# Optimization experiments

Measured on AMD Instinct MI355X. Metric: run time of the kernel, lower is better.

Reference implementation:

```python
import jax, jax.numpy as jnp
import numpy as np

EPS = 1e-4  # softmax_kernel eps

def softmax_kernel(data, projection, is_query):
    # data: [b,h,n,d], projection: [m,d]
    d = data.shape[-1]
    m = projection.shape[0]
    data_normalizer = d ** -0.25
    ratio = m ** -0.5
    data_dash = jnp.einsum('bhnd,md->bhnm', data_normalizer * data, projection)
    diag_data = (jnp.sum(data ** 2, axis=-1) * 0.5 * data_normalizer ** 2)[..., None]  # [b,h,n,1]
    if is_query:
        stab = jnp.max(data_dash, axis=-1, keepdims=True)
    else:
        stab = jnp.max(data_dash)
    return ratio * (jnp.exp(data_dash - diag_data - stab) + EPS)

def linear_attention(q, k, v):
    # q,k: [b,h,n,m]; v: [b,h,n,e]
    k_cumsum = jnp.sum(k, axis=-2)                                  # [b,h,m]
    D_inv = 1.0 / jnp.einsum('bhnm,bhm->bhn', q, k_cumsum)          # [b,h,n]
    context = jnp.einsum('bhnm,bhne->bhme', k, v)                   # [b,h,m,e]
    return jnp.einsum('bhme,bhnm,bhn->bhne', context, q, D_inv)     # [b,h,n,e]

def setup_inputs() -> dict:
    key = jax.random.key(0)
    kq, kk, kv, kp = jax.random.split(key, 4)
    B, H, N, D = 4, 8, 4096, 64
    M = 266  # int(64 * ln(64))
    q = jax.random.normal(kq, (B, H, N, D), dtype=jnp.float32)
    k = jax.random.normal(kk, (B, H, N, D), dtype=jnp.float32)
    v = jax.random.normal(kv, (B, H, N, D), dtype=jnp.float32)
    # Gaussian random-feature projection (stand-in for orthogonal blocks; same math path)
    projection = jax.random.normal(kp, (M, D), dtype=jnp.float32)
    return {"q": q, "k": k, "v": v, "projection": projection}

def reference(q, k, v, projection):
    q_prime = softmax_kernel(q, projection, is_query=True)
    k_prime = softmax_kernel(k, projection, is_query=False)
    return linear_attention(q_prime, k_prime, v)
```

## Files before the change

kernel.cpp:

```cpp
#include <hip/hip_runtime.h>
#include <math.h>

#define NN 4096
#define DD 64
#define MM 266
#define MP 272
#define NORMZ 0.35355339059327379f
#define RATIO 0.06131393394849658f
#define EPSV 1e-4f
#define NEG_INF (-3.4e38f)
#define LSTR 72
#define GSTR 320

typedef __attribute__((ext_vector_type(8))) short bfrag;
typedef __attribute__((ext_vector_type(4))) float f32x4;

#define MFMA(a, b, c) __builtin_amdgcn_mfma_f32_16x16x32_bf16((a), (b), (c), 0, 0, 0)

__device__ inline ushort bf16rne(float x) {
    union { float f; unsigned u; } c; c.f = x;
    unsigned r = c.u + 0x7FFFu + ((c.u >> 16) & 1u);
    return (ushort)(r >> 16);
}
__device__ inline float bf2f(ushort h) {
    union { unsigned u; float f; } c; c.u = ((unsigned)h) << 16;
    return c.f;
}
__device__ inline void splitf(float x, ushort& h, ushort& l) {
    h = bf16rne(x);
    l = bf16rne(x - bf2f(h));
}
__device__ inline void pack8(const float4& a, const float4& b, bfrag& H, bfrag& L) {
    ushort h, l;
    splitf(a.x, h, l); H[0] = (short)h; L[0] = (short)l;
    splitf(a.y, h, l); H[1] = (short)h; L[1] = (short)l;
    splitf(a.z, h, l); H[2] = (short)h; L[2] = (short)l;
    splitf(a.w, h, l); H[3] = (short)h; L[3] = (short)l;
    splitf(b.x, h, l); H[4] = (short)h; L[4] = (short)l;
    splitf(b.y, h, l); H[5] = (short)h; L[5] = (short)l;
    splitf(b.z, h, l); H[6] = (short)h; L[6] = (short)l;
    splitf(b.w, h, l); H[7] = (short)h; L[7] = (short)l;
}

__global__ void proj_split(const float* __restrict__ proj,
                           ushort* __restrict__ pH, ushort* __restrict__ pL)
{
    int i = (blockIdx.x * 256 + threadIdx.x) * 4;
    int m = i >> 6;
    float4 x = (m < MM) ? *(const float4*)(proj + i) : make_float4(0.f, 0.f, 0.f, 0.f);
    ushort h0, l0, h1, l1, h2, l2, h3, l3;
    splitf(x.x, h0, l0); splitf(x.y, h1, l1); splitf(x.z, h2, l2); splitf(x.w, h3, l3);
    *(ushort4*)(pH + i) = make_ushort4(h0, h1, h2, h3);
    *(ushort4*)(pL + i) = make_ushort4(l0, l1, l2, l3);
}

__global__ void reduce_max_kernel(const float* __restrict__ partmax,
                                  float* __restrict__ stab, int n)
{
    __shared__ float sm[256];
    const int t = threadIdx.x;
    float mx = NEG_INF;
    for (int i = t; i < n; i += 256) mx = fmaxf(mx, partmax[i]);
    sm[t] = mx;
    __syncthreads();
    for (int s = 128; s > 0; s >>= 1) {
        if (t < s) sm[t] = fmaxf(sm[t], sm[t + s]);
        __syncthreads();
    }
    if (t == 0) *stab = sm[0];
}

__launch_bounds__(256, 2)
__global__ void kpass(const float* __restrict__ kin, const float* __restrict__ vin,
                      const ushort* __restrict__ pjH, const ushort* __restrict__ pjL,
                      float* __restrict__ ctxP, float* __restrict__ kcP,
                      float* __restrict__ pmax, float* __restrict__ vsum)
{
    __shared__ ushort dataH[64 * LSTR], dataLo[64 * LSTR];
    __shared__ ushort vTH[64 * LSTR], vTLo[64 * LSTR];
    __shared__ ushort r2H[64 * LSTR], r2Lo[64 * LSTR];
    __shared__ float diagS[64];
    __shared__ float kcS[MP];
    __shared__ float redS[4];
    __shared__ float vredS[DD];

    const int t = threadIdx.x;
    const int w = t >> 6;
    const int lane = t & 63;
    const int l15 = lane & 15;
    const int q = lane >> 4;
    const int hd = blockIdx.y;
    const int nb = blockIdx.x;

    kcS[t] = 0.f;
    if (t < 16) kcS[256 + t] = 0.f;
    if (t < DD) vredS[t] = 0.f;

    const f32x4 zf = {0.f, 0.f, 0.f, 0.f};
    f32x4 cacc[4][4];
    f32x4 cacc4 = zf;
    #pragma unroll
    for (int c = 0; c < 4; ++c)
        #pragma unroll
        for (int e = 0; e < 4; ++e) cacc[c][e] = zf;
    float bmaxl = NEG_INF;
    float4 vacc = make_float4(0.f, 0.f, 0.f, 0.f);

    #pragma unroll 1
    for (int st = 0; st < 4; ++st) {
        const int n0 = (nb << 8) + (st << 6);
        __syncthreads();

        const float* kb = kin + ((size_t)hd * NN + n0) * DD;
        #pragma unroll
        for (int j = 0; j < 4; ++j) {
            int i = (t + (j << 8)) << 2;
            int r = i >> 6, cc = i & 63;
            float4 x = *(const float4*)(kb + i);
            float x0 = x.x * NORMZ, x1 = x.y * NORMZ, x2 = x.z * NORMZ, x3 = x.w * NORMZ;
            ushort h0, l0, h1, l1, h2, l2, h3, l3;
            splitf(x0, h0, l0); splitf(x1, h1, l1); splitf(x2, h2, l2); splitf(x3, h3, l3);
            *(ushort4*)&dataH[r * LSTR + cc] = make_ushort4(h0, h1, h2, h3);
            *(ushort4*)&dataLo[r * LSTR + cc] = make_ushort4(l0, l1, l2, l3);
            float ss = x0 * x0 + x1 * x1 + x2 * x2 + x3 * x3;
            #pragma unroll
            for (int d = 1; d < 16; d <<= 1) ss += __shfl_xor(ss, d);
            if (l15 == 0) diagS[r] = 0.5f * ss;
        }
        const float* vb = vin + ((size_t)hd * NN + n0) * DD;
        #pragma unroll
        for (int j = 0; j < 4; ++j) {
            int i = (t + (j << 8)) << 2;
            int n = i >> 6, e = i & 63;
            float4 x = *(const float4*)(vb + i);
            vacc.x += x.x; vacc.y += x.y; vacc.z += x.z; vacc.w += x.w;
            ushort h, l;
            splitf(x.x, h, l); vTH[(e + 0) * LSTR + n] = h; vTLo[(e + 0) * LSTR + n] = l;
            splitf(x.y, h, l); vTH[(e + 1) * LSTR + n] = h; vTLo[(e + 1) * LSTR + n] = l;
            splitf(x.z, h, l); vTH[(e + 2) * LSTR + n] = h; vTLo[(e + 2) * LSTR + n] = l;
            splitf(x.w, h, l); vTH[(e + 3) * LSTR + n] = h; vTLo[(e + 3) * LSTR + n] = l;
        }
        __syncthreads();

        bfrag aH[2], aL[2];
        {
            const int row = (w << 4) + l15;
            aH[0] = *(const bfrag*)&dataH[row * LSTR + (q << 3)];
            aH[1] = *(const bfrag*)&dataH[row * LSTR + 32 + (q << 3)];
            aL[0] = *(const bfrag*)&dataLo[row * LSTR + (q << 3)];
            aL[1] = *(const bfrag*)&dataLo[row * LSTR + 32 + (q << 3)];
        }

        #pragma unroll
        for (int c = 0; c < 5; ++c) {
            const int mtiles = (c < 4) ? 4 : 1;
            const int m0 = c << 6;
            {
                const int tot = mtiles << 7;
                for (int idx = t; idx < tot; idx += 256) {
                    int i = idx << 3; int r = i >> 6, cc = i & 63;
                    *(uint4*)&r2H[r * LSTR + cc] = *(const uint4*)(pjH + ((m0 + r) << 6) + cc);
                    *(uint4*)&r2Lo[r * LSTR + cc] = *(const uint4*)(pjL + ((m0 + r) << 6) + cc);
                }
            }
            __syncthreads();

            f32x4 dd4[4];
            #pragma unroll
            for (int mt = 0; mt < 4; ++mt) {
                if (mt >= mtiles) break;
                const int mrow = (mt << 4) + l15;
                bfrag bH0 = *(const bfrag*)&r2H[mrow * LSTR + (q << 3)];
                bfrag bH1 = *(const bfrag*)&r2H[mrow * LSTR + 32 + (q << 3)];
                bfrag bL0 = *(const bfrag*)&r2Lo[mrow * LSTR + (q << 3)];
                bfrag bL1 = *(const bfrag*)&r2Lo[mrow * LSTR + 32 + (q << 3)];
                f32x4 a = zf;
                a = MFMA(aH[0], bL0, a);
                a = MFMA(aH[1], bL1, a);
                a = MFMA(aL[0], bH0, a);
                a = MFMA(aL[1], bH1, a);
                a = MFMA(aH[0], bH0, a);
                a = MFMA(aH[1], bH1, a);
                dd4[mt] = a;
            }
            #pragma unroll
            for (int mt = 0; mt < 4; ++mt) {
                if (mt >= mtiles) break;
                const int mg = m0 + (mt << 4) + l15;
                const bool valid = (mg < MM);
                ushort uh[4], ul[4];
                float csum = 0.f;
                #pragma unroll
                for (int reg = 0; reg < 4; ++reg) {
                    float dv = dd4[mt][reg];
                    float u = 0.f;
                    if (valid) {
                        bmaxl = fmaxf(bmaxl, dv);
                        u = __expf(dv - diagS[(w << 4) + (q << 2) + reg]);
                    }
                    csum += u;
                    splitf(u, uh[reg], ul[reg]);
                }
                *(ushort4*)&dataH[((mt << 4) + l15) * LSTR + (w << 4) + (q << 2)] =
                    make_ushort4(uh[0], uh[1], uh[2], uh[3]);
                *(ushort4*)&dataLo[((mt << 4) + l15) * LSTR + (w << 4) + (q << 2)] =
                    make_ushort4(ul[0], ul[1], ul[2], ul[3]);
                csum += __shfl_xor(csum, 16);
                csum += __shfl_xor(csum, 32);
                if (q == 0) atomicAdd(&kcS[mg], csum);
            }
            __syncthreads();

            if (c < 4) {
                const int mrow = (w << 4) + l15;
                bfrag uH0 = *(const bfrag*)&dataH[mrow * LSTR + (q << 3)];
                bfrag uH1 = *(const bfrag*)&dataH[mrow * LSTR + 32 + (q << 3)];
                bfrag uL0 = *(const bfrag*)&dataLo[mrow * LSTR + (q << 3)];
                bfrag uL1 = *(const bfrag*)&dataLo[mrow * LSTR + 32 + (q << 3)];
                #pragma unroll
                for (int et = 0; et < 4; ++et) {
                    const int erow = (et << 4) + l15;
                    bfrag vH0 = *(const bfrag*)&vTH[erow * LSTR + (q << 3)];
                    bfrag vH1 = *(const bfrag*)&vTH[erow * LSTR + 32 + (q << 3)];
                    bfrag vL0 = *(const bfrag*)&vTLo[erow * LSTR + (q << 3)];
                    bfrag vL1 = *(const bfrag*)&vTLo[erow * LSTR + 32 + (q << 3)];
                    f32x4 a = cacc[c][et];
                    a = MFMA(uH0, vL0, a);
                    a = MFMA(uH1, vL1, a);
                    a = MFMA(uL0, vH0, a);
                    a = MFMA(uL1, vH1, a);
                    a = MFMA(uH0, vH0, a);
                    a = MFMA(uH1, vH1, a);
                    cacc[c][et] = a;
                }
            } else {
                const int mrow = l15;
                bfrag uH0 = *(const bfrag*)&dataH[mrow * LSTR + (q << 3)];
                bfrag uH1 = *(const bfrag*)&dataH[mrow * LSTR + 32 + (q << 3)];
                bfrag uL0 = *(const bfrag*)&dataLo[mrow * LSTR + (q << 3)];
                bfrag uL1 = *(const bfrag*)&dataLo[mrow * LSTR + 32 + (q << 3)];
                const int erow = (w << 4) + l15;
                bfrag vH0 = *(const bfrag*)&vTH[erow * LSTR + (q << 3)];
                bfrag vH1 = *(const bfrag*)&vTH[erow * LSTR + 32 + (q << 3)];
                bfrag vL0 = *(const bfrag*)&vTLo[erow * LSTR + (q << 3)];
                bfrag vL1 = *(const bfrag*)&vTLo[erow * LSTR + 32 + (q << 3)];
                f32x4 a = cacc4;
                a = MFMA(uH0, vL0, a);
                a = MFMA(uH1, vL1, a);
                a = MFMA(uL0, vH0, a);
                a = MFMA(uL1, vH1, a);
                a = MFMA(uH0, vH0, a);
                a = MFMA(uH1, vH1, a);
                cacc4 = a;
            }
        }
    }

    __syncthreads();
    {
        float bm = bmaxl;
        #pragma unroll
        for (int d = 1; d < 64; d <<= 1) bm = fmaxf(bm, __shfl_xor(bm, d));
        if (lane == 0) redS[w] = bm;
    }
    {
        const int e0 = (t << 2) & 63;
        atomicAdd(&vredS[e0 + 0], vacc.x);
        atomicAdd(&vredS[e0 + 1], vacc.y);
        atomicAdd(&vredS[e0 + 2], vacc.z);
        atomicAdd(&vredS[e0 + 3], vacc.w);
    }
    __syncthreads();
    if (t == 0) pmax[hd * 16 + nb] = fmaxf(fmaxf(redS[0], redS[1]), fmaxf(redS[2], redS[3]));
    if (t < DD) atomicAdd(&vsum[hd * DD + t], vredS[t]);
    for (int m = t; m < MP; m += 256) kcP[(size_t)(hd * 16 + nb) * MP + m] = kcS[m];
    float* cp = ctxP + (size_t)(hd * 16 + nb) * MP * DD;
    #pragma unroll
    for (int c = 0; c < 4; ++c) {
        const int mbase = (c << 6) + (w << 4) + (q << 2);
        #pragma unroll
        for (int et = 0; et < 4; ++et)
            #pragma unroll
            for (int reg = 0; reg < 4; ++reg)
                cp[(mbase + reg) * DD + (et << 4) + l15] = cacc[c][et][reg];
    }
    #pragma unroll
    for (int reg = 0; reg < 4; ++reg)
        cp[(256 + (q << 2) + reg) * DD + (w << 4) + l15] = cacc4[reg];
}

__global__ void ctx_reduce(const float* __restrict__ ctxP, const float* __restrict__ kcP,
                           const float* __restrict__ vsum, const float* __restrict__ stabp,
                           ushort* __restrict__ gH, ushort* __restrict__ gL,
                           float* __restrict__ kcF)
{
    __shared__ ushort hiT[64][20], loT[64][20];
    const int t = threadIdx.x, mt = blockIdx.x, hd = blockIdx.y;
    const float Asc = RATIO * __expf(-*stabp);
    const float REPS = RATIO * EPSV;
    const int e = t & 63, mq = t >> 6;
    const float vs = vsum[hd * DD + e];
    #pragma unroll
    for (int i = 0; i < 4; ++i) {
        const int ml = mq * 4 + i;
        const int m = mt * 16 + ml;
        float s = 0.f;
        for (int nbk = 0; nbk < 16; ++nbk)
            s += ctxP[((size_t)(hd * 16 + nbk) * MP + m) * DD + e];
        float val = Asc * s + REPS * vs;
        ushort h, l; splitf(val, h, l);
        hiT[e][ml] = h; loT[e][ml] = l;
    }
    __syncthreads();
    {
        const int i = t * 4, e2 = i >> 4, cc = i & 15;
        ushort4 hv = make_ushort4(hiT[e2][cc], hiT[e2][cc + 1], hiT[e2][cc + 2], hiT[e2][cc + 3]);
        ushort4 lv = make_ushort4(loT[e2][cc], loT[e2][cc + 1], loT[e2][cc + 2], loT[e2][cc + 3]);
        *(ushort4*)(gH + ((size_t)hd * 64 + e2) * GSTR + mt * 16 + cc) = hv;
        *(ushort4*)(gL + ((size_t)hd * 64 + e2) * GSTR + mt * 16 + cc) = lv;
    }
    if (t < 16) {
        const int m = mt * 16 + t;
        float s = 0.f;
        for (int nbk = 0; nbk < 16; ++nbk) s += kcP[(size_t)(hd * 16 + nbk) * MP + m];
        kcF[hd * MP + m] = Asc * s + ((m < MM) ? REPS * (float)NN : 0.f);
    }
}

__launch_bounds__(256, 4)
__global__ void qpass(const float* __restrict__ qin,
                      const ushort* __restrict__ pjH, const ushort* __restrict__ pjL,
                      const ushort* __restrict__ gH, const ushort* __restrict__ gL,
                      const float* __restrict__ kcF,
                      float* __restrict__ outp)
{
    __shared__ ushort bPH[64 * LSTR], bPL[64 * LSTR];
    __shared__ ushort bQH[64 * LSTR], bQL[64 * LSTR];

    const int t = threadIdx.x;
    const int w = t >> 6;
    const int lane = t & 63;
    const int l15 = lane & 15;
    const int q = lane >> 4;
    const int hd = blockIdx.y;
    const int n0 = blockIdx.x << 6;

    const float* qb = qin + ((size_t)hd * NN + n0) * DD;
    const int row = (w << 4) + l15;
    float4 x0 = *(const float4*)(qb + (row << 6) + (q << 3));
    float4 x1 = *(const float4*)(qb + (row << 6) + (q << 3) + 4);
    float4 x2 = *(const float4*)(qb + (row << 6) + 32 + (q << 3));
    float4 x3 = *(const float4*)(qb + (row << 6) + 32 + (q << 3) + 4);
    x0.x *= NORMZ; x0.y *= NORMZ; x0.z *= NORMZ; x0.w *= NORMZ;
    x1.x *= NORMZ; x1.y *= NORMZ; x1.z *= NORMZ; x1.w *= NORMZ;
    x2.x *= NORMZ; x2.y *= NORMZ; x2.z *= NORMZ; x2.w *= NORMZ;
    x3.x *= NORMZ; x3.y *= NORMZ; x3.z *= NORMZ; x3.w *= NORMZ;
    float ss = x0.x*x0.x + x0.y*x0.y + x0.z*x0.z + x0.w*x0.w
             + x1.x*x1.x + x1.y*x1.y + x1.z*x1.z + x1.w*x1.w
             + x2.x*x2.x + x2.y*x2.y + x2.z*x2.z + x2.w*x2.w
             + x3.x*x3.x + x3.y*x3.y + x3.z*x3.z + x3.w*x3.w;
    ss += __shfl_xor(ss, 16);
    ss += __shfl_xor(ss, 32);
    float dg[4];
    #pragma unroll
    for (int r = 0; r < 4; ++r) dg[r] = 0.5f * __shfl(ss, (q << 2) + r);
    bfrag aH[2], aL[2];
    pack8(x0, x1, aH[0], aL[0]);
    pack8(x2, x3, aH[1], aL[1]);

    const f32x4 zf = {0.f, 0.f, 0.f, 0.f};
    f32x4 ddq[17];

    #pragma unroll
    for (int c = 0; c < 5; ++c) {
        const int mtiles = (c < 4) ? 4 : 1;
        const int m0 = c << 6;
        __syncthreads();
        {
            const int tot = mtiles << 7;
            for (int idx = t; idx < tot; idx += 256) {
                int i = idx << 3; int r = i >> 6, cc = i & 63;
                *(uint4*)&bPH[r * LSTR + cc] = *(const uint4*)(pjH + ((m0 + r) << 6) + cc);
                *(uint4*)&bPL[r * LSTR + cc] = *(const uint4*)(pjL + ((m0 + r) << 6) + cc);
            }
        }
        __syncthreads();
        #pragma unroll
        for (int mt = 0; mt < 4; ++mt) {
            if (mt >= mtiles) break;
            const int mrow = (mt << 4) + l15;
            bfrag bH0 = *(const bfrag*)&bPH[mrow * LSTR + (q << 3)];
            bfrag bH1 = *(const bfrag*)&bPH[mrow * LSTR + 32 + (q << 3)];
            bfrag bL0 = *(const bfrag*)&bPL[mrow * LSTR + (q << 3)];
            bfrag bL1 = *(const bfrag*)&bPL[mrow * LSTR + 32 + (q << 3)];
            f32x4 a = zf;
            a = MFMA(aH[0], bL0, a);
            a = MFMA(aH[1], bL1, a);
            a = MFMA(aL[0], bH0, a);
            a = MFMA(aL[1], bH1, a);
            a = MFMA(aH[0], bH0, a);
            a = MFMA(aH[1], bH1, a);
            ddq[c * 4 + mt] = a;
        }
    }

    float rmax[4];
    #pragma unroll
    for (int reg = 0; reg < 4; ++reg) {
        float mx = NEG_INF;
        #pragma unroll
        for (int ti = 0; ti < 17; ++ti) {
            bool valid = (ti < 16) || (l15 < 10);
            if (valid) mx = fmaxf(mx, ddq[ti][reg]);
        }
        #pragma unroll
        for (int d = 1; d < 16; d <<= 1) mx = fmaxf(mx, __shfl_xor(mx, d));
        rmax[reg] = mx;
    }
    #pragma unroll
    for (int ti = 0; ti < 17; ++ti) {
        #pragma unroll
        for (int reg = 0; reg < 4; ++reg) {
            bool valid = (ti < 16) || (l15 < 10);
            float e = 0.f;
            if (valid)
                e = RATIO * (__expf(ddq[ti][reg] - dg[reg] - rmax[reg]) + EPSV);
            ddq[ti][reg] = e;
        }
    }
    float dinv[4];
    {
        const float* kcb = kcF + hd * MP;
        float den[4] = {0.f, 0.f, 0.f, 0.f};
        #pragma unroll
        for (int ti = 0; ti < 17; ++ti) {
            float kv = kcb[(ti << 4) + l15];
            #pragma unroll
            for (int reg = 0; reg < 4; ++reg) den[reg] += ddq[ti][reg] * kv;
        }
        #pragma unroll
        for (int reg = 0; reg < 4; ++reg) {
            #pragma unroll
            for (int d = 1; d < 16; d <<= 1) den[reg] += __shfl_xor(den[reg], d);
            dinv[reg] = 1.f / den[reg];
        }
    }

    f32x4 oacc[4];
    #pragma unroll
    for (int et = 0; et < 4; ++et) oacc[et] = zf;

    #pragma unroll
    for (int c = 0; c < 5; ++c) {
        const int mtiles = (c < 4) ? 4 : 1;
        __syncthreads();
        #pragma unroll
        for (int mt = 0; mt < 4; ++mt) {
            if (mt >= mtiles) break;
            const int ml = (mt << 4) + l15;
            #pragma unroll
            for (int reg = 0; reg < 4; ++reg) {
                ushort h, l; splitf(ddq[c * 4 + mt][reg], h, l);
                bPH[((w << 4) + (q << 2) + reg) * LSTR + ml] = h;
                bPL[((w << 4) + (q << 2) + reg) * LSTR + ml] = l;
            }
        }
        if (c == 4) {
            const int rown = (w << 4) + l15;
            *(ushort4*)&bPH[rown * LSTR + 16 + (q << 2)] = make_ushort4(0, 0, 0, 0);
            *(ushort4*)&bPL[rown * LSTR + 16 + (q << 2)] = make_ushort4(0, 0, 0, 0);
        }
        {
            for (int idx = t; idx < 512; idx += 256) {
                int i = idx << 3; int e = i >> 6, mm = i & 63;
                *(uint4*)&bQH[e * LSTR + mm] =
                    *(const uint4*)(gH + ((size_t)hd * 64 + e) * GSTR + (c << 6) + mm);
                *(uint4*)&bQL[e * LSTR + mm] =
                    *(const uint4*)(gL + ((size_t)hd * 64 + e) * GSTR + (c << 6) + mm);
            }
        }
        __syncthreads();
        const int arow = (w << 4) + l15;
        bfrag pH0 = *(const bfrag*)&bPH[arow * LSTR + (q << 3)];
        bfrag pL0 = *(const bfrag*)&bPL[arow * LSTR + (q << 3)];
        bfrag pH1, pL1;
        if (c < 4) {
            pH1 = *(const bfrag*)&bPH[arow * LSTR + 32 + (q << 3)];
            pL1 = *(const bfrag*)&bPL[arow * LSTR + 32 + (q << 3)];
        }
        #pragma unroll
        for (int et = 0; et < 4; ++et) {
            const int erow = (et << 4) + l15;
            bfrag cH0 = *(const bfrag*)&bQH[erow * LSTR + (q << 3)];
            bfrag cL0 = *(const bfrag*)&bQL[erow * LSTR + (q << 3)];
            f32x4 a = oacc[et];
            a = MFMA(pH0, cL0, a);
            a = MFMA(pL0, cH0, a);
            a = MFMA(pH0, cH0, a);
            if (c < 4) {
                bfrag cH1 = *(const bfrag*)&bQH[erow * LSTR + 32 + (q << 3)];
                bfrag cL1 = *(const bfrag*)&bQL[erow * LSTR + 32 + (q << 3)];
                a = MFMA(pH1, cL1, a);
                a = MFMA(pL1, cH1, a);
                a = MFMA(pH1, cH1, a);
            }
            oacc[et] = a;
        }
    }

    float* ob = outp + ((size_t)hd * NN + n0) * DD;
    #pragma unroll
    for (int et = 0; et < 4; ++et)
        #pragma unroll
        for (int reg = 0; reg < 4; ++reg)
            ob[((w << 4) + (q << 2) + reg) * DD + (et << 4) + l15] = oacc[et][reg] * dinv[reg];
}

extern "C" void kernel_launch(void* const* d_in, const int* in_sizes, int n_in,
                              void* d_out, int out_size, void* d_ws, size_t ws_size,
                              hipStream_t stream)
{
    const float* q = (const float*)d_in[0];
    const float* k = (const float*)d_in[1];
    const float* v = (const float*)d_in[2];
    const float* proj = (const float*)d_in[3];
    float* out = (float*)d_out;
    char* ws = (char*)d_ws;

    ushort* gH  = (ushort*)(ws);
    ushort* gL  = (ushort*)(ws + 1310720);
    float*  vsm = (float*)(ws + 2621440);
    ushort* pH  = (ushort*)(ws + 2629632);
    ushort* pL  = (ushort*)(ws + 2664448);
    float*  kcF = (float*)(ws + 2699264);
    float*  ctxP= (float*)(ws + 2734080);
    float*  kcP = (float*)(ws + 38385664);
    float*  pmax= (float*)(ws + 38942720);
    float*  stab= (float*)(ws + 38944768);

    hipMemsetAsync(ws, 0, 2629632, stream);

    proj_split<<<dim3(17), 256, 0, stream>>>(proj, pH, pL);
    kpass<<<dim3(16, 32), 256, 0, stream>>>(k, v, pH, pL, ctxP, kcP, pmax, vsm);
    reduce_max_kernel<<<1, 256, 0, stream>>>(pmax, stab, 512);
    ctx_reduce<<<dim3(17, 32), 256, 0, stream>>>(ctxP, kcP, vsm, stab, gH, gL, kcF);
    qpass<<<dim3(64, 32), 256, 0, stream>>>(q, pH, pL, gH, gL, kcF, out);
}
```

Measured before the change: 256.6 us.

## Double kpass block to 512 threads, splitting m/e tiles across wave halves

```diff
diff --git a/kernel.cpp b/kernel.cpp
--- a/kernel.cpp
+++ b/kernel.cpp
@@ -70,7 +70,7 @@
     if (t == 0) *stab = sm[0];
 }
 
-__launch_bounds__(256, 2)
+__launch_bounds__(512, 4)
 __global__ void kpass(const float* __restrict__ kin, const float* __restrict__ vin,
                       const ushort* __restrict__ pjH, const ushort* __restrict__ pjL,
                       float* __restrict__ ctxP, float* __restrict__ kcP,
@@ -81,7 +81,7 @@
     __shared__ ushort r2H[64 * LSTR], r2Lo[64 * LSTR];
     __shared__ float diagS[64];
     __shared__ float kcS[MP];
-    __shared__ float redS[4];
+    __shared__ float redS[8];
     __shared__ float vredS[DD];
 
     const int t = threadIdx.x;
@@ -89,20 +89,21 @@
     const int lane = t & 63;
     const int l15 = lane & 15;
     const int q = lane >> 4;
+    const int s = w & 3;
+    const int h = w >> 2;
     const int hd = blockIdx.y;
     const int nb = blockIdx.x;
 
-    kcS[t] = 0.f;
-    if (t < 16) kcS[256 + t] = 0.f;
+    if (t < MP) kcS[t] = 0.f;
     if (t < DD) vredS[t] = 0.f;
 
     const f32x4 zf = {0.f, 0.f, 0.f, 0.f};
-    f32x4 cacc[4][4];
+    f32x4 cacc[4][2];
     f32x4 cacc4 = zf;
     #pragma unroll
     for (int c = 0; c < 4; ++c)
         #pragma unroll
-        for (int e = 0; e < 4; ++e) cacc[c][e] = zf;
+        for (int e = 0; e < 2; ++e) cacc[c][e] = zf;
     float bmaxl = NEG_INF;
     float4 vacc = make_float4(0.f, 0.f, 0.f, 0.f);
 
@@ -113,8 +114,8 @@
 
         const float* kb = kin + ((size_t)hd * NN + n0) * DD;
         #pragma unroll
-        for (int j = 0; j < 4; ++j) {
-            int i = (t + (j << 8)) << 2;
+        for (int j = 0; j < 2; ++j) {
+            int i = (t + (j << 9)) << 2;
             int r = i >> 6, cc = i & 63;
             float4 x = *(const float4*)(kb + i);
             float x0 = x.x * NORMZ, x1 = x.y * NORMZ, x2 = x.z * NORMZ, x3 = x.w * NORMZ;
@@ -129,22 +130,22 @@
         }
         const float* vb = vin + ((size_t)hd * NN + n0) * DD;
         #pragma unroll
-        for (int j = 0; j < 4; ++j) {
-            int i = (t + (j << 8)) << 2;
+        for (int j = 0; j < 2; ++j) {
+            int i = (t + (j << 9)) << 2;
             int n = i >> 6, e = i & 63;
             float4 x = *(const float4*)(vb + i);
             vacc.x += x.x; vacc.y += x.y; vacc.z += x.z; vacc.w += x.w;
-            ushort h, l;
-            splitf(x.x, h, l); vTH[(e + 0) * LSTR + n] = h; vTLo[(e + 0) * LSTR + n] = l;
-            splitf(x.y, h, l); vTH[(e + 1) * LSTR + n] = h; vTLo[(e + 1) * LSTR + n] = l;
-            splitf(x.z, h, l); vTH[(e + 2) * LSTR + n] = h; vTLo[(e + 2) * LSTR + n] = l;
-            splitf(x.w, h, l); vTH[(e + 3) * LSTR + n] = h; vTLo[(e + 3) * LSTR + n] = l;
+            ushort hh, ll;
+            splitf(x.x, hh, ll); vTH[(e + 0) * LSTR + n] = hh; vTLo[(e + 0) * LSTR + n] = ll;
+            splitf(x.y, hh, ll); vTH[(e + 1) * LSTR + n] = hh; vTLo[(e + 1) * LSTR + n] = ll;
+            splitf(x.z, hh, ll); vTH[(e + 2) * LSTR + n] = hh; vTLo[(e + 2) * LSTR + n] = ll;
+            splitf(x.w, hh, ll); vTH[(e + 3) * LSTR + n] = hh; vTLo[(e + 3) * LSTR + n] = ll;
         }
         __syncthreads();
 
         bfrag aH[2], aL[2];
         {
-            const int row = (w << 4) + l15;
+            const int row = (s << 4) + l15;
             aH[0] = *(const bfrag*)&dataH[row * LSTR + (q << 3)];
             aH[1] = *(const bfrag*)&dataH[row * LSTR + 32 + (q << 3)];
             aL[0] = *(const bfrag*)&dataLo[row * LSTR + (q << 3)];
@@ -157,7 +158,7 @@
             const int m0 = c << 6;
             {
                 const int tot = mtiles << 7;
-                for (int idx = t; idx < tot; idx += 256) {
+                for (int idx = t; idx < tot; idx += 512) {
                     int i = idx << 3; int r = i >> 6, cc = i & 63;
                     *(uint4*)&r2H[r * LSTR + cc] = *(const uint4*)(pjH + ((m0 + r) << 6) + cc);
                     *(uint4*)&r2Lo[r * LSTR + cc] = *(const uint4*)(pjL + ((m0 + r) << 6) + cc);
@@ -165,9 +166,10 @@
             }
             __syncthreads();
 
-            f32x4 dd4[4];
-            #pragma unroll
-            for (int mt = 0; mt < 4; ++mt) {
+            f32x4 dd4[2];
+            #pragma unroll
+            for (int m2 = 0; m2 < 2; ++m2) {
+                const int mt = (h << 1) + m2;
                 if (mt >= mtiles) break;
                 const int mrow = (mt << 4) + l15;
                 bfrag bH0 = *(const bfrag*)&r2H[mrow * LSTR + (q << 3)];
@@ -181,10 +183,11 @@
                 a = MFMA(aL[1], bH1, a);
                 a = MFMA(aH[0], bH0, a);
                 a = MFMA(aH[1], bH1, a);
-                dd4[mt] = a;
-            }
-            #pragma unroll
-            for (int mt = 0; mt < 4; ++mt) {
+                dd4[m2] = a;
+            }
+            #pragma unroll
+            for (int m2 = 0; m2 < 2; ++m2) {
+                const int mt = (h << 1) + m2;
                 if (mt >= mtiles) break;
                 const int mg = m0 + (mt << 4) + l15;
                 const bool valid = (mg < MM);
@@ -192,18 +195,18 @@
                 float csum = 0.f;
                 #pragma unroll
                 for (int reg = 0; reg < 4; ++reg) {
-                    float dv = dd4[mt][reg];
+                    float dv = dd4[m2][reg];
                     float u = 0.f;
                     if (valid) {
                         bmaxl = fmaxf(bmaxl, dv);
-                        u = __expf(dv - diagS[(w << 4) + (q << 2) + reg]);
+                        u = __expf(dv - diagS[(s << 4) + (q << 2) + reg]);
                     }
                     csum += u;
                     splitf(u, uh[reg], ul[reg]);
                 }
-                *(ushort4*)&dataH[((mt << 4) + l15) * LSTR + (w << 4) + (q << 2)] =
+                *(ushort4*)&dataH[((mt << 4) + l15) * LSTR + (s << 4) + (q << 2)] =
                     make_ushort4(uh[0], uh[1], uh[2], uh[3]);
-                *(ushort4*)&dataLo[((mt << 4) + l15) * LSTR + (w << 4) + (q << 2)] =
+                *(ushort4*)&dataLo[((mt << 4) + l15) * LSTR + (s << 4) + (q << 2)] =
                     make_ushort4(ul[0], ul[1], ul[2], ul[3]);
                 csum += __shfl_xor(csum, 16);
                 csum += __shfl_xor(csum, 32);
@@ -212,28 +215,29 @@
             __syncthreads();
 
             if (c < 4) {
-                const int mrow = (w << 4) + l15;
+                const int mrow = (s << 4) + l15;
                 bfrag uH0 = *(const bfrag*)&dataH[mrow * LSTR + (q << 3)];
                 bfrag uH1 = *(const bfrag*)&dataH[mrow * LSTR + 32 + (q << 3)];
                 bfrag uL0 = *(const bfrag*)&dataLo[mrow * LSTR + (q << 3)];
                 bfrag uL1 = *(const bfrag*)&dataLo[mrow * LSTR + 32 + (q << 3)];
                 #pragma unroll
-                for (int et = 0; et < 4; ++et) {
+                for (int e2 = 0; e2 < 2; ++e2) {
+                    const int et = (h << 1) + e2;
                     const int erow = (et << 4) + l15;
                     bfrag vH0 = *(const bfrag*)&vTH[erow * LSTR + (q << 3)];
                     bfrag vH1 = *(const bfrag*)&vTH[erow * LSTR + 32 + (q << 3)];
                     bfrag vL0 = *(const bfrag*)&vTLo[erow * LSTR + (q << 3)];
                     bfrag vL1 = *(const bfrag*)&vTLo[erow * LSTR + 32 + (q << 3)];
-                    f32x4 a = cacc[c][et];
+                    f32x4 a = cacc[c][e2];
                     a = MFMA(uH0, vL0, a);
                     a = MFMA(uH1, vL1, a);
                     a = MFMA(uL0, vH0, a);
                     a = MFMA(uL1, vH1, a);
                     a = MFMA(uH0, vH0, a);
                     a = MFMA(uH1, vH1, a);
-                    cacc[c][et] = a;
+                    cacc[c][e2] = a;
                 }
-            } else {
+            } else if (w < 4) {
                 const int mrow = l15;
                 bfrag uH0 = *(const bfrag*)&dataH[mrow * LSTR + (q << 3)];
                 bfrag uH1 = *(const bfrag*)&dataH[mrow * LSTR + 32 + (q << 3)];
@@ -271,22 +275,31 @@
         atomicAdd(&vredS[e0 + 3], vacc.w);
     }
     __syncthreads();
-    if (t == 0) pmax[hd * 16 + nb] = fmaxf(fmaxf(redS[0], redS[1]), fmaxf(redS[2], redS[3]));
+    if (t == 0) {
+        float bm = redS[0];
+        #pragma unroll
+        for (int i = 1; i < 8; ++i) bm = fmaxf(bm, redS[i]);
+        pmax[hd * 16 + nb] = bm;
+    }
     if (t < DD) atomicAdd(&vsum[hd * DD + t], vredS[t]);
-    for (int m = t; m < MP; m += 256) kcP[(size_t)(hd * 16 + nb) * MP + m] = kcS[m];
+    for (int m = t; m < MP; m += 512) kcP[(size_t)(hd * 16 + nb) * MP + m] = kcS[m];
     float* cp = ctxP + (size_t)(hd * 16 + nb) * MP * DD;
     #pragma unroll
     for (int c = 0; c < 4; ++c) {
-        const int mbase = (c << 6) + (w << 4) + (q << 2);
-        #pragma unroll
-        for (int et = 0; et < 4; ++et)
+        const int mbase = (c << 6) + (s << 4) + (q << 2);
+        #pragma unroll
+        for (int e2 = 0; e2 < 2; ++e2) {
+            const int et = (h << 1) + e2;
             #pragma unroll
             for (int reg = 0; reg < 4; ++reg)
-                cp[(mbase + reg) * DD + (et << 4) + l15] = cacc[c][et][reg];
-    }
-    #pragma unroll
-    for (int reg = 0; reg < 4; ++reg)
-        cp[(256 + (q << 2) + reg) * DD + (w << 4) + l15] = cacc4[reg];
+                cp[(mbase + reg) * DD + (et << 4) + l15] = cacc[c][e2][reg];
+        }
+    }
+    if (w < 4) {
+        #pragma unroll
+        for (int reg = 0; reg < 4; ++reg)
+            cp[(256 + (q << 2) + reg) * DD + (w << 4) + l15] = cacc4[reg];
+    }
 }
 
 __global__ void ctx_reduce(const float* __restrict__ ctxP, const float* __restrict__ kcP,
@@ -460,9 +473,9 @@
             const int ml = (mt << 4) + l15;
             #pragma unroll
             for (int reg = 0; reg < 4; ++reg) {
-                ushort h, l; splitf(ddq[c * 4 + mt][reg], h, l);
-                bPH[((w << 4) + (q << 2) + reg) * LSTR + ml] = h;
-                bPL[((w << 4) + (q << 2) + reg) * LSTR + ml] = l;
+                ushort hh, ll; splitf(ddq[c * 4 + mt][reg], hh, ll);
+                bPH[((w << 4) + (q << 2) + reg) * LSTR + ml] = hh;
+                bPL[((w << 4) + (q << 2) + reg) * LSTR + ml] = ll;
             }
         }
         if (c == 4) {
@@ -541,7 +554,7 @@
     hipMemsetAsync(ws, 0, 2629632, stream);
 
     proj_split<<<dim3(17), 256, 0, stream>>>(proj, pH, pL);
-    kpass<<<dim3(16, 32), 256, 0, stream>>>(k, v, pH, pL, ctxP, kcP, pmax, vsm);
+    kpass<<<dim3(16, 32), 512, 0, stream>>>(k, v, pH, pL, ctxP, kcP, pmax, vsm);
     reduce_max_kernel<<<1, 256, 0, stream>>>(pmax, stab, 512);
     ctx_reduce<<<dim3(17, 32), 256, 0, stream>>>(ctxP, kcP, vsm, stab, gH, gL, kcF);
     qpass<<<dim3(64, 32), 256, 0, stream>>>(q, pH, pL, gH, gL, kcF, out);
```

Result: slower. 282.9 us (+10.3%).
